# Performance work log

Hardware: AMD Instinct MI355X
Metric: run time of the kernel (lower is better)

The kernel has to match this reference:

```python
import jax, jax.numpy as jnp
import numpy as np

D = 69      # input_size = 54 dofs + 15 actions
E = 132     # time2vec embedding
R = 1024    # rnn_size
B = 2048    # batch
S = 50      # source_seq_len
T = 25      # target_seq_len


def setup_inputs() -> dict:
    key = jax.random.key(0)
    ks = jax.random.split(key, 18)
    w = lambda k, shape: jax.random.normal(k, shape, jnp.float32) * 0.05
    return dict(
        encoder_inputs=jax.random.normal(ks[0], (B, S - 1, D), jnp.float32),
        decoder_inputs=jax.random.normal(ks[1], (B, T, D), jnp.float32),
        noise=jax.random.normal(ks[2], (B, R), jnp.float32),
        Wih_enc=w(ks[3], (4 * R, D + E)), Whh_enc=w(ks[4], (4 * R, R)),
        bih_enc=w(ks[5], (4 * R,)), bhh_enc=w(ks[6], (4 * R,)),
        Wih_dec=w(ks[7], (4 * R, D)), Whh_dec=w(ks[8], (4 * R, R)),
        bih_dec=w(ks[9], (4 * R,)), bhh_dec=w(ks[10], (4 * R,)),
        fc1_w=w(ks[11], (D, R)), fc1_b=w(ks[12], (D,)),
        mu_w=w(ks[13], (1, R)), mu_b=w(ks[14], (1,)),
        sigma_w=w(ks[15], (1, R)), sigma_b=jnp.ones((1,), jnp.float32),  # bias 1 keeps sigma away from 0
        t2v_w=w(ks[16], (E, D)), t2v_b=w(ks[17], (E,)),
    )


def _lstm_step(x, h, c, Wih, Whh, bih, bhh):
    # PyTorch LSTMCell gate order: i, f, g, o
    gates = x @ Wih.T + bih + h @ Whh.T + bhh
    i, f, g, o = jnp.split(gates, 4, axis=-1)
    c = jax.nn.sigmoid(f) * c + jax.nn.sigmoid(i) * jnp.tanh(g)
    h = jax.nn.sigmoid(o) * jnp.tanh(c)
    return h, c


def _forward(encoder_inputs, decoder_inputs, noise,
             Wih_enc, Whh_enc, bih_enc, bhh_enc,
             Wih_dec, Whh_dec, bih_dec, bhh_dec,
             fc1_w, fc1_b, mu_w, mu_b, sigma_w, sigma_b, t2v_w, t2v_b):
    batch = encoder_inputs.shape[0]
    # time2vec embedding + concat: [B, S-1, D+E]
    emb = jnp.sin(encoder_inputs @ t2v_w.T + t2v_b)
    enc_seq = jnp.swapaxes(jnp.concatenate([encoder_inputs, emb], axis=2), 0, 1)
    h0 = jnp.zeros((batch, R), encoder_inputs.dtype)
    c0 = jnp.zeros((batch, R), encoder_inputs.dtype)

    def enc_step(carry, x):
        h, c = carry
        h, c = _lstm_step(x, h, c, Wih_enc, Whh_enc, bih_enc, bhh_enc)
        return (h, c), None  # dropout is identity in eval mode

    (h, c), _ = jax.lax.scan(enc_step, (h0, c0), enc_seq)

    mu = h @ mu_w.T + mu_b          # [B, 1]
    sigma = c @ sigma_w.T + sigma_b  # [B, 1]
    h = (h - mu) / sigma
    c = (c - mu) / sigma
    # eval-mode stochastic perturbation (same noise added to both, as in torch)
    h = h + 10.0 * noise
    c = c + 10.0 * noise

    dec_seq = jnp.swapaxes(decoder_inputs, 0, 1)  # [T, B, D]

    def dec_step(carry, x):
        h, c = carry
        h, c = _lstm_step(x, h, c, Wih_dec, Whh_dec, bih_dec, bhh_dec)
        out = x + h @ fc1_w.T + fc1_b  # residual projection
        return (h, c), out

    _, outs = jax.lax.scan(dec_step, (h, c), dec_seq)  # [T, B, D]
    return jnp.swapaxes(outs, 0, 1)  # [B, T, D]


def reference(encoder_inputs, decoder_inputs, noise,
              Wih_enc, Whh_enc, bih_enc, bhh_enc,
              Wih_dec, Whh_dec, bih_dec, bhh_dec,
              fc1_w, fc1_b, mu_w, mu_b, sigma_w, sigma_b, t2v_w, t2v_b):
    return _forward(encoder_inputs, decoder_inputs, noise,
                    Wih_enc, Whh_enc, bih_enc, bhh_enc,
                    Wih_dec, Whh_dec, bih_dec, bhh_dec,
                    fc1_w, fc1_b, mu_w, mu_b, sigma_w, sigma_b, t2v_w, t2v_b)
```

## Files before the change

### kernel.cpp

```cpp
#include <hip/hip_runtime.h>
#include <hip/hip_bf16.h>
#include <math.h>

#define DI 69
#define EE 132
#define RR 1024
#define BB 2048
#define TT 25
#define SE 49

typedef _Float16 f16;
typedef _Float16 v8h __attribute__((ext_vector_type(8)));
typedef float f32x4 __attribute__((ext_vector_type(4)));

__device__ __forceinline__ float sigm(float x) { return 1.0f / (1.0f + __expf(-x)); }
__device__ __forceinline__ float tanhf_fast(float x) {
  float e = __expf(2.0f * x);
  return 1.0f - 2.0f / (e + 1.0f);
}

typedef const __attribute__((address_space(1))) char* gas1p;
typedef __attribute__((address_space(3))) char* las3p;
__device__ __forceinline__ void gld16(const void* g, void* l) {
  __builtin_amdgcn_global_load_lds((gas1p)g, (las3p)l, 16, 0, 0);
}



__global__ void prep_misc_kernel(float* __restrict__ c, f16* __restrict__ h0,
                                 const float* __restrict__ bih_e, const float* __restrict__ bhh_e,
                                 const float* __restrict__ bih_d, const float* __restrict__ bhh_d,
                                 float* __restrict__ bias_e, float* __restrict__ bias_d,
                                 const float* __restrict__ fc1_w, f16* __restrict__ fc1h,
                                 const float* __restrict__ t2v_w, f16* __restrict__ wt2)
{
  int i = blockIdx.x * 256 + threadIdx.x;
  if (i < BB * RR) { c[i] = 0.0f; h0[i] = (f16)0.0f; }
  if (i < 4096) { bias_e[i] = bih_e[i] + bhh_e[i]; bias_d[i] = bih_d[i] + bhh_d[i]; }
  if (i < 128 * RR) {
    int dr = i >> 10, k = i & 1023;
    int kd = k ^ ((dr & 7) << 3);
    fc1h[(dr << 10) | kd] = (f16)((dr < DI) ? fc1_w[dr * RR + k] : 0.0f);
  }
  if (i < 160 * 128) {
    int r = i >> 7, k = i & 127;
    float v = (r < EE && k < DI) ? t2v_w[r * DI + k] : 0.0f;
    wt2[(r << 7) | (k ^ ((r & 7) << 3))] = (f16)v;
  }
}

__global__ void prep_wq_kernel(const float* __restrict__ Whh, const float* __restrict__ Wih,
                               f16* __restrict__ Wq, int KT, int DIN)
{
  int j = blockIdx.x;
  int xo = (j & 7) << 3;
  for (int k = threadIdx.x; k < KT; k += blockDim.x) {
    float v;
    if (k < RR) v = Whh[(size_t)j * RR + k];
    else { int kk = k - RR; v = (kk < DIN) ? Wih[(size_t)j * DIN + kk] : 0.0f; }
    Wq[(size_t)j * KT + (k ^ xo)] = (f16)v;
  }
}

__global__ void xf16_kernel(const float* __restrict__ enc_in,
                            f16* __restrict__ Xf, f16* __restrict__ feat)
{
  int idx = blockIdx.x * 256 + threadIdx.x;
  if (idx >= SE * BB * 256) return;
  int j = idx & 255, row = idx >> 8;
  int t = row >> 11, b = row & (BB - 1);
  int xo = (b & 7) << 3;
  int k = j ^ xo;
  if (k < 128) {
    float v = (k < DI) ? enc_in[(size_t)b * SE * DI + t * DI + k] : 0.0f;
    Xf[(size_t)row * 128 + j] = (f16)v;
    if (k < DI) feat[(size_t)row * 256 + j] = (f16)v;
  } else if (k >= 201) {
    feat[(size_t)row * 256 + j] = (f16)0.0f;
  }
}

__global__ __launch_bounds__(256)
void t2v_kernel(const f16* __restrict__ Xf, const f16* __restrict__ wt2,
                const float* __restrict__ t2v_b, f16* __restrict__ feat)
{
  __shared__ __align__(16) f16 lA[128 * 64];
  __shared__ __align__(16) f16 lB[160 * 64];
  __shared__ float bl[EE];
  const int tid = threadIdx.x;
  const int m0 = blockIdx.x * 128;
  const int lane = tid & 63, w = tid >> 6;
  const int lrow = lane & 15;
  const int r8 = lane >> 3, s8 = lane & 7;
  if (tid < EE) bl[tid] = t2v_b[tid];

  f32x4 acc[2][10];
  #pragma unroll
  for (int a = 0; a < 2; ++a)
    #pragma unroll
    for (int n = 0; n < 10; ++n) acc[a][n] = (f32x4){0.f, 0.f, 0.f, 0.f};

  const int sw0 = (((lane >> 4)) ^ s8) * 8;
  const int sw1 = (((lane >> 4) | 4) ^ s8) * 8;

  for (int kt = 0; kt < 2; ++kt) {
    __syncthreads();
    #pragma unroll
    for (int i = 0; i < 4; ++i)
      gld16(Xf + (size_t)(m0 + w * 32 + 8 * i + r8) * 128 + kt * 64 + s8 * 8,
            &lA[(w * 32 + 8 * i) * 64]);
    #pragma unroll
    for (int i = 0; i < 5; ++i)
      gld16(wt2 + (size_t)(w * 40 + 8 * i + r8) * 128 + kt * 64 + s8 * 8,
            &lB[(w * 40 + 8 * i) * 64]);
    __syncthreads();
    v8h av0[2], av1[2];
    #pragma unroll
    for (int mf = 0; mf < 2; ++mf) {
      av0[mf] = *(const v8h*)(&lA[(w * 32 + mf * 16 + lrow) * 64 + sw0]);
      av1[mf] = *(const v8h*)(&lA[(w * 32 + mf * 16 + lrow) * 64 + sw1]);
    }
    #pragma unroll
    for (int nf = 0; nf < 10; ++nf) {
      v8h bv0 = *(const v8h*)(&lB[(nf * 16 + lrow) * 64 + sw0]);
      v8h bv1 = *(const v8h*)(&lB[(nf * 16 + lrow) * 64 + sw1]);
      #pragma unroll
      for (int mf = 0; mf < 2; ++mf) {
        acc[mf][nf] = __builtin_amdgcn_mfma_f32_16x16x32_f16(av0[mf], bv0, acc[mf][nf], 0, 0, 0);
        acc[mf][nf] = __builtin_amdgcn_mfma_f32_16x16x32_f16(av1[mf], bv1, acc[mf][nf], 0, 0, 0);
      }
    }
  }
  #pragma unroll
  for (int nf = 0; nf < 10; ++nf) {
    int e = nf * 16 + lrow;
    if (e < EE) {
      float be = bl[e];
      #pragma unroll
      for (int mf = 0; mf < 2; ++mf) {
        int rbase = m0 + w * 32 + mf * 16 + (lane >> 4) * 4;
        #pragma unroll
        for (int q = 0; q < 4; ++q) {
          int row = rbase + q;
          feat[(size_t)row * 256 + ((69 + e) ^ ((row & 7) << 3))]
              = (f16)__sinf(acc[mf][nf][q] + be);
        }
      }
    }
  }
}

__global__ void feat_dec_kernel(const float* __restrict__ dec_in, f16* __restrict__ feat)
{
  int idx = blockIdx.x * 256 + threadIdx.x;
  if (idx >= TT * BB * 128) return;
  int k = idx & 127;
  int r = idx >> 7;
  int t = r >> 11, b = r & (BB - 1);
  float v = (k < DI) ? dec_in[(size_t)b * TT * DI + t * DI + k] : 0.0f;
  feat[((size_t)r << 7) | (k ^ ((b & 7) << 3))] = (f16)v;
}

template<int FT, int FPAD, bool WF32>
__global__ __launch_bounds__(256, 2)
void lstm_step_kernel(const f16* __restrict__ hin, const f16* __restrict__ feat,
                      const f16* __restrict__ Wq, const float* __restrict__ bias,
                      float* __restrict__ c, f16* __restrict__ hout,
                      float* __restrict__ hf32)
{
  constexpr int KT = (16 + FT) * 64;
  __shared__ __align__(16) f16 lA[128 * 64];
  __shared__ __align__(16) f16 lB[128 * 64];
  const int tid = threadIdx.x;
  const int m0 = blockIdx.y * 128;
  const int u0 = blockIdx.x * 32;
  const int lane = tid & 63, w = tid >> 6;
  const int wm = w >> 1, wn = w & 1;
  const int lrow = lane & 15;
  const int r8 = lane >> 3, s8 = lane & 7;

  const f16* pA[4]; const f16* pB[4];
  f16* dA[4]; f16* dB[4];
  #pragma unroll
  for (int i = 0; i < 4; ++i) {
    int rA = w * 32 + 8 * i;
    dA[i] = lA + rA * 64;
    dB[i] = lB + rA * 64;
    pA[i] = hin + (size_t)(m0 + rA + r8) * RR + s8 * 8;
    pB[i] = Wq + (size_t)(w * 1024 + u0 + 8 * i + r8) * KT + s8 * 8;
  }

  f32x4 acc[4][4];
  #pragma unroll
  for (int a = 0; a < 4; ++a)
    #pragma unroll
    for (int g = 0; g < 4; ++g) acc[a][g] = (f32x4){0.f, 0.f, 0.f, 0.f};

  const int sw0 = (((lane >> 4)) ^ s8) * 8;
  const int sw1 = (((lane >> 4) | 4) ^ s8) * 8;
  const f16* a0 = lA + (wm * 64 + lrow) * 64 + sw0;
  const f16* a1 = lA + (wm * 64 + lrow) * 64 + sw1;
  const f16* b0 = lB + (wn * 16 + lrow) * 64 + sw0;
  const f16* b1 = lB + (wn * 16 + lrow) * 64 + sw1;

  for (int kt = 0; kt < 16 + FT; ++kt) {
    if (kt == 16) {
      #pragma unroll
      for (int i = 0; i < 4; ++i)
        pA[i] = feat + (size_t)(m0 + w * 32 + 8 * i + r8) * FPAD + s8 * 8;
    }
    #pragma unroll
    for (int i = 0; i < 4; ++i) { gld16(pA[i], dA[i]); pA[i] += 64; }
    #pragma unroll
    for (int i = 0; i < 4; ++i) { gld16(pB[i], dB[i]); pB[i] += 64; }
    __syncthreads();

    v8h av0[4], av1[4], bv0[4], bv1[4];
    #pragma unroll
    for (int mf = 0; mf < 4; ++mf) {
      av0[mf] = *(const v8h*)(a0 + mf * 1024);
      av1[mf] = *(const v8h*)(a1 + mf * 1024);
    }
    #pragma unroll
    for (int g = 0; g < 4; ++g) {
      bv0[g] = *(const v8h*)(b0 + g * 2048);
      bv1[g] = *(const v8h*)(b1 + g * 2048);
    }
    #pragma unroll
    for (int mf = 0; mf < 4; ++mf)
      #pragma unroll
      for (int g = 0; g < 4; ++g) {
        acc[mf][g] = __builtin_amdgcn_mfma_f32_16x16x32_f16(av0[mf], bv0[g], acc[mf][g], 0, 0, 0);
        acc[mf][g] = __builtin_amdgcn_mfma_f32_16x16x32_f16(av1[mf], bv1[g], acc[mf][g], 0, 0, 0);
      }
    __syncthreads();
  }

  const int u = u0 + wn * 16 + lrow;
  const float bi = bias[u], bf = bias[1024 + u], bg = bias[2048 + u], bo = bias[3072 + u];
  #pragma unroll
  for (int mf = 0; mf < 4; ++mf) {
    int rbase = m0 + wm * 64 + mf * 16 + (lane >> 4) * 4;
    #pragma unroll
    for (int q = 0; q < 4; ++q) {
      int r = rbase + q;
      size_t idxc = (size_t)r * RR + u;
      float iv = acc[mf][0][q] + bi;
      float fv = acc[mf][1][q] + bf;
      float gv = acc[mf][2][q] + bg;
      float ov = acc[mf][3][q] + bo;
      float cn = sigm(fv) * c[idxc] + sigm(iv) * tanhf_fast(gv);
      float hn = sigm(ov) * tanhf_fast(cn);
      c[idxc] = cn;
      hout[(size_t)r * RR + (u ^ ((r & 7) << 3))] = (f16)hn;
      if (WF32) hf32[idxc] = hn;
    }
  }
}

__global__ void musigma_kernel(const float* __restrict__ hf, float* __restrict__ c,
                               const float* __restrict__ noise,
                               const float* __restrict__ mu_w, const float* __restrict__ mu_b,
                               const float* __restrict__ sig_w, const float* __restrict__ sig_b,
                               f16* __restrict__ hout)
{
  int b = blockIdx.x, tid = threadIdx.x;
  __shared__ float red[8];
  __shared__ float musig[2];
  float sh = 0.f, sc = 0.f;
  for (int k = tid; k < RR; k += 256) {
    size_t idx = (size_t)b * RR + k;
    sh += hf[idx] * mu_w[k];
    sc += c[idx] * sig_w[k];
  }
  for (int off = 32; off > 0; off >>= 1) { sh += __shfl_down(sh, off); sc += __shfl_down(sc, off); }
  int wid = tid >> 6;
  if ((tid & 63) == 0) { red[wid] = sh; red[4 + wid] = sc; }
  __syncthreads();
  if (tid == 0) {
    musig[0] = red[0] + red[1] + red[2] + red[3] + mu_b[0];
    musig[1] = red[4] + red[5] + red[6] + red[7] + sig_b[0];
  }
  __syncthreads();
  float mu = musig[0], sg = musig[1];
  int xo = (b & 7) << 3;
  for (int k = tid; k < RR; k += 256) {
    size_t idx = (size_t)b * RR + k;
    float n10 = 10.0f * noise[idx];
    float hh = (hf[idx] - mu) / sg + n10;
    float cc = (c[idx] - mu) / sg + n10;
    hout[(size_t)b * RR + (k ^ xo)] = (f16)hh;
    c[idx] = cc;
  }
}

__global__ __launch_bounds__(256, 2)
void final_fc_kernel(const f16* __restrict__ Hd, const f16* __restrict__ fw,
                     const float* __restrict__ fb, const float* __restrict__ dec_in,
                     float* __restrict__ out)
{
  __shared__ __align__(16) f16 lA[128 * 64];
  __shared__ __align__(16) f16 lB[128 * 64];
  const int tid = threadIdx.x;
  const int m0 = blockIdx.x * 128;
  const int lane = tid & 63, w = tid >> 6;
  const int lrow = lane & 15;
  const int r8 = lane >> 3, s8 = lane & 7;

  const f16* pA[4]; const f16* pB[4];
  f16* dA[4]; f16* dB[4];
  #pragma unroll
  for (int i = 0; i < 4; ++i) {
    int rA = w * 32 + 8 * i;
    dA[i] = lA + rA * 64;
    dB[i] = lB + rA * 64;
    pA[i] = Hd + (size_t)(m0 + rA + r8) * RR + s8 * 8;
    pB[i] = fw + (size_t)(rA + r8) * RR + s8 * 8;
  }

  f32x4 acc[2][5];
  #pragma unroll
  for (int a = 0; a < 2; ++a)
    #pragma unroll
    for (int n = 0; n < 5; ++n) acc[a][n] = (f32x4){0.f, 0.f, 0.f, 0.f};

  const int sw0 = (((lane >> 4)) ^ s8) * 8;
  const int sw1 = (((lane >> 4) | 4) ^ s8) * 8;
  const f16* a0 = lA + (w * 32 + lrow) * 64 + sw0;
  const f16* a1 = lA + (w * 32 + lrow) * 64 + sw1;
  const f16* b0 = lB + lrow * 64 + sw0;
  const f16* b1 = lB + lrow * 64 + sw1;

  for (int kt = 0; kt < 16; ++kt) {
    #pragma unroll
    for (int i = 0; i < 4; ++i) { gld16(pA[i], dA[i]); pA[i] += 64; }
    #pragma unroll
    for (int i = 0; i < 4; ++i) { gld16(pB[i], dB[i]); pB[i] += 64; }
    __syncthreads();
    v8h av0[2], av1[2], bv0[5], bv1[5];
    #pragma unroll
    for (int mf = 0; mf < 2; ++mf) {
      av0[mf] = *(const v8h*)(a0 + mf * 1024);
      av1[mf] = *(const v8h*)(a1 + mf * 1024);
    }
    #pragma unroll
    for (int nf = 0; nf < 5; ++nf) {
      bv0[nf] = *(const v8h*)(b0 + nf * 1024);
      bv1[nf] = *(const v8h*)(b1 + nf * 1024);
    }
    #pragma unroll
    for (int mf = 0; mf < 2; ++mf)
      #pragma unroll
      for (int nf = 0; nf < 5; ++nf) {
        acc[mf][nf] = __builtin_amdgcn_mfma_f32_16x16x32_f16(av0[mf], bv0[nf], acc[mf][nf], 0, 0, 0);
        acc[mf][nf] = __builtin_amdgcn_mfma_f32_16x16x32_f16(av1[mf], bv1[nf], acc[mf][nf], 0, 0, 0);
      }
    __syncthreads();
  }
  #pragma unroll
  for (int mf = 0; mf < 2; ++mf) {
    int rbase = m0 + w * 32 + mf * 16 + (lane >> 4) * 4;
    #pragma unroll
    for (int nf = 0; nf < 5; ++nf) {
      int col = nf * 16 + lrow;
      if (col < DI) {
        #pragma unroll
        for (int q = 0; q < 4; ++q) {
          int m = rbase + q;
          int t = m >> 11, b = m & (BB - 1);
          size_t oi = (size_t)b * TT * DI + t * DI + col;
          out[oi] = acc[mf][nf][q] + fb[col] + dec_in[oi];
        }
      }
    }
  }
}

extern "C" void kernel_launch(void* const* d_in, const int* in_sizes, int n_in,
                              void* d_out, int out_size, void* d_ws, size_t ws_size,
                              hipStream_t stream)
{
  const float* enc_in = (const float*)d_in[0];
  const float* dec_in = (const float*)d_in[1];
  const float* noise  = (const float*)d_in[2];
  const float* Wih_e  = (const float*)d_in[3];
  const float* Whh_e  = (const float*)d_in[4];
  const float* bih_e  = (const float*)d_in[5];
  const float* bhh_e  = (const float*)d_in[6];
  const float* Wih_d  = (const float*)d_in[7];
  const float* Whh_d  = (const float*)d_in[8];
  const float* bih_d  = (const float*)d_in[9];
  const float* bhh_d  = (const float*)d_in[10];
  const float* fc1_w  = (const float*)d_in[11];
  const float* fc1_b  = (const float*)d_in[12];
  const float* mu_w   = (const float*)d_in[13];
  const float* mu_b   = (const float*)d_in[14];
  const float* sig_w  = (const float*)d_in[15];
  const float* sig_b  = (const float*)d_in[16];
  const float* t2v_w  = (const float*)d_in[17];
  const float* t2v_b  = (const float*)d_in[18];
  float* outp = (float*)d_out;

  char* ws = (char*)d_ws;
  size_t off = 0;
  auto alloc = [&](size_t bytes) -> char* {
    char* p = ws + off; off += (bytes + 255) & ~(size_t)255; return p;
  };
  f16*   wq_e   = (f16*)alloc((size_t)4096 * 1280 * 2);
  f16*   wq_d   = (f16*)alloc((size_t)4096 * 1152 * 2);
  f16*   fc1h   = (f16*)alloc((size_t)128 * RR * 2);
  f16*   wt2    = (f16*)alloc((size_t)160 * 128 * 2);
  float* bias_e = (float*)alloc(4096 * 4);
  float* bias_d = (float*)alloc(4096 * 4);
  f16*   feat_e = (f16*)alloc((size_t)SE * BB * 256 * 2);
  f16*   feat_d = (f16*)alloc((size_t)TT * BB * 128 * 2);
  f16*   h_ping = (f16*)alloc((size_t)BB * RR * 2);
  f16*   h_pong = (f16*)alloc((size_t)BB * RR * 2);
  float* cbuf   = (float*)alloc((size_t)BB * RR * 4);
  float* hf32   = (float*)alloc((size_t)BB * RR * 4);
  f16*   Hd     = (f16*)alloc((size_t)TT * BB * RR * 2);
  if (off > ws_size) return;
  f16*   Xf     = Hd;

  prep_misc_kernel<<<(BB * RR + 255) / 256, 256, 0, stream>>>(
      cbuf, h_ping, bih_e, bhh_e, bih_d, bhh_d, bias_e, bias_d, fc1_w, fc1h, t2v_w, wt2);
  prep_wq_kernel<<<4096, 256, 0, stream>>>(Whh_e, Wih_e, wq_e, 1280, DI + EE);
  prep_wq_kernel<<<4096, 256, 0, stream>>>(Whh_d, Wih_d, wq_d, 1152, DI);
  xf16_kernel<<<(SE * BB * 256 + 255) / 256, 256, 0, stream>>>(enc_in, Xf, feat_e);
  t2v_kernel<<<SE * (BB / 128), 256, 0, stream>>>(Xf, wt2, t2v_b, feat_e);
  feat_dec_kernel<<<(TT * BB * 128 + 255) / 256, 256, 0, stream>>>(dec_in, feat_d);

  dim3 sgrid(32, 16, 1);

  f16* hcur = h_ping; f16* hnxt = h_pong;
  for (int t = 0; t < SE; ++t) {
    const f16* ft = feat_e + (size_t)t * BB * 256;
    if (t == SE - 1)
      lstm_step_kernel<4, 256, true><<<sgrid, 256, 0, stream>>>(
          hcur, ft, wq_e, bias_e, cbuf, hnxt, hf32);
    else
      lstm_step_kernel<4, 256, false><<<sgrid, 256, 0, stream>>>(
          hcur, ft, wq_e, bias_e, cbuf, hnxt, nullptr);
    f16* tmp = hcur; hcur = hnxt; hnxt = tmp;
  }

  musigma_kernel<<<BB, 256, 0, stream>>>(hf32, cbuf, noise, mu_w, mu_b, sig_w, sig_b, h_ping);

  const f16* din = h_ping;
  for (int t = 0; t < TT; ++t) {
    f16* hout = Hd + (size_t)t * BB * RR;
    lstm_step_kernel<2, 128, false><<<sgrid, 256, 0, stream>>>(
        din, feat_d + (size_t)t * BB * 128, wq_d, bias_d, cbuf, hout, nullptr);
    din = hout;
  }

  final_fc_kernel<<<(TT * BB) / 128, 256, 0, stream>>>(Hd, fc1h, fc1_b, dec_in, outp);
}
```

Before: 2.294 ms.

## Double-buffer LDS tiles in LSTM step GEMM and vectorize input conversion

The LSTM step kernel now keeps two LDS buffers for the A and B tiles. It issues global-to-LDS loads two stages ahead, using explicit vmcnt waits and barriers, so memory transfer overlaps with the MFMA work. This doubles LDS use per block to 64 KB, which may limit occupancy at two blocks per CU. The xf16 conversion kernel is also rewritten so each thread handles 8 elements and writes them as 16-byte vectors, including the zero padding.

Measured after the change: 2.220 ms. -3.2%, faster.

```diff
diff --git a/kernel.cpp b/kernel.cpp
--- a/kernel.cpp
+++ b/kernel.cpp
@@ -66,17 +66,28 @@
                             f16* __restrict__ Xf, f16* __restrict__ feat)
 {
   int idx = blockIdx.x * 256 + threadIdx.x;
-  if (idx >= SE * BB * 256) return;
-  int j = idx & 255, row = idx >> 8;
+  if (idx >= SE * BB * 32) return;
+  int m = idx & 31, row = idx >> 5;
   int t = row >> 11, b = row & (BB - 1);
   int xo = (b & 7) << 3;
-  int k = j ^ xo;
-  if (k < 128) {
-    float v = (k < DI) ? enc_in[(size_t)b * SE * DI + t * DI + k] : 0.0f;
-    Xf[(size_t)row * 128 + j] = (f16)v;
-    if (k < DI) feat[(size_t)row * 256 + j] = (f16)v;
-  } else if (k >= 201) {
-    feat[(size_t)row * 256 + j] = (f16)0.0f;
+  int c0 = m * 8;
+  if (m <= 8) {
+    const float* src = enc_in + ((size_t)b * SE + t) * DI + c0;
+    f16 v[8];
+    #pragma unroll
+    for (int e = 0; e < 8; ++e) v[e] = (f16)((c0 + e < DI) ? src[e] : 0.0f);
+    *(v8h*)(Xf + (size_t)row * 128 + (c0 ^ xo)) = *(v8h*)v;
+    *(v8h*)(feat + (size_t)row * 256 + (c0 ^ xo)) = *(v8h*)v;
+  } else if (m <= 15) {
+    v8h z = {};
+    *(v8h*)(Xf + (size_t)row * 128 + (c0 ^ xo)) = z;
+  } else if (m == 25) {
+    #pragma unroll
+    for (int e = 1; e < 8; ++e)
+      feat[(size_t)row * 256 + ((200 + e) ^ xo)] = (f16)0.0f;
+  } else if (m >= 26) {
+    v8h z = {};
+    *(v8h*)(feat + (size_t)row * 256 + (c0 ^ xo)) = z;
   }
 }
 
@@ -168,9 +179,10 @@
                       float* __restrict__ c, f16* __restrict__ hout,
                       float* __restrict__ hf32)
 {
-  constexpr int KT = (16 + FT) * 64;
-  __shared__ __align__(16) f16 lA[128 * 64];
-  __shared__ __align__(16) f16 lB[128 * 64];
+  constexpr int NIT = 16 + FT;
+  constexpr int KT = NIT * 64;
+  __shared__ __align__(16) f16 lA[2][128 * 64];
+  __shared__ __align__(16) f16 lB[2][128 * 64];
   const int tid = threadIdx.x;
   const int m0 = blockIdx.y * 128;
   const int u0 = blockIdx.x * 32;
@@ -179,14 +191,12 @@
   const int lrow = lane & 15;
   const int r8 = lane >> 3, s8 = lane & 7;
 
-  const f16* pA[4]; const f16* pB[4];
-  f16* dA[4]; f16* dB[4];
+  const f16* pAh[4]; const f16* pAf[4]; const f16* pB[4];
   #pragma unroll
   for (int i = 0; i < 4; ++i) {
     int rA = w * 32 + 8 * i;
-    dA[i] = lA + rA * 64;
-    dB[i] = lB + rA * 64;
-    pA[i] = hin + (size_t)(m0 + rA + r8) * RR + s8 * 8;
+    pAh[i] = hin + (size_t)(m0 + rA + r8) * RR + s8 * 8;
+    pAf[i] = feat + (size_t)(m0 + rA + r8) * FPAD + s8 * 8;
     pB[i] = Wq + (size_t)(w * 1024 + u0 + 8 * i + r8) * KT + s8 * 8;
   }
 
@@ -198,33 +208,33 @@
 
   const int sw0 = (((lane >> 4)) ^ s8) * 8;
   const int sw1 = (((lane >> 4) | 4) ^ s8) * 8;
-  const f16* a0 = lA + (wm * 64 + lrow) * 64 + sw0;
-  const f16* a1 = lA + (wm * 64 + lrow) * 64 + sw1;
-  const f16* b0 = lB + (wn * 16 + lrow) * 64 + sw0;
-  const f16* b1 = lB + (wn * 16 + lrow) * 64 + sw1;
-
-  for (int kt = 0; kt < 16 + FT; ++kt) {
-    if (kt == 16) {
-      #pragma unroll
-      for (int i = 0; i < 4; ++i)
-        pA[i] = feat + (size_t)(m0 + w * 32 + 8 * i + r8) * FPAD + s8 * 8;
-    }
-    #pragma unroll
-    for (int i = 0; i < 4; ++i) { gld16(pA[i], dA[i]); pA[i] += 64; }
-    #pragma unroll
-    for (int i = 0; i < 4; ++i) { gld16(pB[i], dB[i]); pB[i] += 64; }
-    __syncthreads();
-
+  const int oa = (wm * 64 + lrow) * 64;
+  const int ob = (wn * 16 + lrow) * 64;
+
+  auto STAGE = [&](int s) {
+    int buf = s & 1;
+    #pragma unroll
+    for (int i = 0; i < 4; ++i) {
+      const f16* src = (s < 16) ? (pAh[i] + s * 64) : (pAf[i] + (s - 16) * 64);
+      gld16(src, &lA[buf][(w * 32 + 8 * i) * 64]);
+    }
+    #pragma unroll
+    for (int i = 0; i < 4; ++i)
+      gld16(pB[i] + s * 64, &lB[buf][(w * 32 + 8 * i) * 64]);
+  };
+  auto COMPUTE = [&](int buf) {
+    const f16* Ab = &lA[buf][oa];
+    const f16* Bb = &lB[buf][ob];
     v8h av0[4], av1[4], bv0[4], bv1[4];
     #pragma unroll
     for (int mf = 0; mf < 4; ++mf) {
-      av0[mf] = *(const v8h*)(a0 + mf * 1024);
-      av1[mf] = *(const v8h*)(a1 + mf * 1024);
+      av0[mf] = *(const v8h*)(Ab + mf * 1024 + sw0);
+      av1[mf] = *(const v8h*)(Ab + mf * 1024 + sw1);
     }
     #pragma unroll
     for (int g = 0; g < 4; ++g) {
-      bv0[g] = *(const v8h*)(b0 + g * 2048);
-      bv1[g] = *(const v8h*)(b1 + g * 2048);
+      bv0[g] = *(const v8h*)(Bb + g * 2048 + sw0);
+      bv1[g] = *(const v8h*)(Bb + g * 2048 + sw1);
     }
     #pragma unroll
     for (int mf = 0; mf < 4; ++mf)
@@ -233,8 +243,21 @@
         acc[mf][g] = __builtin_amdgcn_mfma_f32_16x16x32_f16(av0[mf], bv0[g], acc[mf][g], 0, 0, 0);
         acc[mf][g] = __builtin_amdgcn_mfma_f32_16x16x32_f16(av1[mf], bv1[g], acc[mf][g], 0, 0, 0);
       }
-    __syncthreads();
-  }
+  };
+
+  STAGE(0); STAGE(1);
+
+  for (int kt = 0; kt < NIT - 1; ++kt) {
+    asm volatile("s_waitcnt vmcnt(8)" ::: "memory");
+    __builtin_amdgcn_s_barrier();
+    COMPUTE(kt & 1);
+    asm volatile("s_waitcnt lgkmcnt(0)" ::: "memory");
+    __builtin_amdgcn_s_barrier();
+    if (kt + 2 < NIT) STAGE(kt + 2);
+  }
+  asm volatile("s_waitcnt vmcnt(0)" ::: "memory");
+  __builtin_amdgcn_s_barrier();
+  COMPUTE((NIT - 1) & 1);
 
   const int u = u0 + wn * 16 + lrow;
   const float bi = bias[u], bf = bias[1024 + u], bg = bias[2048 + u], bo = bias[3072 + u];
@@ -426,7 +449,7 @@
       cbuf, h_ping, bih_e, bhh_e, bih_d, bhh_d, bias_e, bias_d, fc1_w, fc1h, t2v_w, wt2);
   prep_wq_kernel<<<4096, 256, 0, stream>>>(Whh_e, Wih_e, wq_e, 1280, DI + EE);
   prep_wq_kernel<<<4096, 256, 0, stream>>>(Whh_d, Wih_d, wq_d, 1152, DI);
-  xf16_kernel<<<(SE * BB * 256 + 255) / 256, 256, 0, stream>>>(enc_in, Xf, feat_e);
+  xf16_kernel<<<(SE * BB * 32 + 255) / 256, 256, 0, stream>>>(enc_in, Xf, feat_e);
   t2v_kernel<<<SE * (BB / 128), 256, 0, stream>>>(Xf, wt2, t2v_b, feat_e);
   feat_dec_kernel<<<(TT * BB * 128 + 255) / 256, 256, 0, stream>>>(dec_in, feat_d);
 
```
